# Kernel tuning notes

Measured on AMD Instinct MI355X. Metric: run time of the kernel, lower is better.

The kernel has to match this reference:

```python
import jax, jax.numpy as jnp
import numpy as np

B, C, W, H = 1024, 1, 128, 128
NUM_IDS = 64
MARGIN = 0.3


def setup_inputs() -> dict:
    key = jax.random.key(0)
    k1, k2 = jax.random.split(key)
    inputs = jax.random.normal(k1, (B, C, W, H), dtype=jnp.float32)
    targets = jax.random.randint(k2, (B,), 0, NUM_IDS, dtype=jnp.int32)
    return {"inputs": inputs, "targets": targets}


def _dc_align(anchor, other):
    # Batched cross-attention alignment (DCModuleOptimized assumption):
    # modi = softmax(anchor @ other^T / sqrt(h)) @ other, per sample.
    h = anchor.shape[-1]
    scale = 1.0 / jnp.sqrt(jnp.asarray(h, anchor.dtype))
    att = jax.nn.softmax(jnp.einsum('bij,bkj->bik', anchor, other) * scale, axis=-1)
    return jnp.einsum('bik,bkj->bij', att, other)


def reference(inputs, targets):
    b, c, w, h = inputs.shape
    x = inputs.reshape(b, -1)                      # (n, d); requires c == 1 downstream
    n = b
    # Pairwise Euclidean distances, stable clamp as in torch code
    sq = jnp.sum(x * x, axis=1)                    # (n,)
    dist = sq[:, None] + sq[None, :] - 2.0 * (x @ x.T)
    dist = jnp.sqrt(jnp.clip(dist, 1e-12, None))   # (n, n)
    mask = targets[:, None] == targets[None, :]    # (n, n) same-identity mask
    # Vectorized hard mining (replaces the per-row Python loop)
    NEG = jnp.asarray(-1e30, dist.dtype)
    POS = jnp.asarray(1e30, dist.dtype)
    hp_idx = jnp.argmax(jnp.where(mask, dist, NEG), axis=1)   # hardest positive per row
    hn_idx = jnp.argmin(jnp.where(mask, POS, dist), axis=1)   # hardest negative per row
    anchor = x.reshape(b, w, h)
    h_pos = anchor[hp_idx]                         # (b, w, h) gathered hard positives
    h_neg = anchor[hn_idx]                         # (b, w, h) gathered hard negatives
    # DC module applied over the whole batch at once
    modi_pos = _dc_align(anchor, h_pos)
    modi_neg = _dc_align(anchor, h_neg)
    dap = anchor.reshape(b, -1) - modi_pos.reshape(b, -1)
    dan = anchor.reshape(b, -1) - modi_neg.reshape(b, -1)
    dist_ap = jnp.sqrt(jnp.sum(dap * dap, axis=1))
    dist_an = jnp.sqrt(jnp.sum(dan * dan, axis=1))
    # MarginRankingLoss with y = 1: mean(relu(dist_ap - dist_an + margin))
    loss = jnp.mean(jax.nn.relu(dist_ap - dist_an + MARGIN))
    return loss
```

## Files before the change

kernel.cpp:

```cpp
#include <hip/hip_runtime.h>
#include <stdint.h>

#define NSAMP 1024
#define D 16384
#define WH 128
#define MARGIN 0.3f
#define SCALE 0.08838834764831845f
#define RSCALE 11.313708498984761f
#define MARG 0.03f
#define LISTCAP 2048

typedef unsigned int uint;
typedef unsigned short ushort_t;

typedef __attribute__((ext_vector_type(8))) short bf16x8;
typedef __attribute__((ext_vector_type(4))) float f32x4;

__device__ __forceinline__ float bf2f(unsigned short b) {
    return __uint_as_float(((uint)b) << 16);
}
__device__ __forceinline__ unsigned short f2bf(float f) {
    uint u = __float_as_uint(f);
    u += 0x7fffu + ((u >> 16) & 1u);
    return (unsigned short)(u >> 16);
}
__device__ __forceinline__ void gload_lds16(const void* g, void* l) {
    __builtin_amdgcn_global_load_lds(
        (const __attribute__((address_space(1))) uint32_t*)g,
        (__attribute__((address_space(3))) uint32_t*)l, 16, 0, 0);
}
__device__ __forceinline__ int lds_off(int row, int col) {
    return row * 256 + ((((col >> 3) ^ (row & 15)) << 4) | ((col & 7) << 1));
}

__global__ __launch_bounds__(256) void k_norms_hi(const float* __restrict__ x,
                                                  float* __restrict__ sq,
                                                  ushort_t* __restrict__ xhi) {
    int b = blockIdx.x;
    int tid = threadIdx.x;
    const float* xr = x + (size_t)b * D;
    ushort_t* hr = xhi + (size_t)b * D;
    float s = 0.f;
    #pragma unroll
    for (int m = 0; m < 16; ++m) {
        int e = m * 1024 + tid * 4;
        float4 v = *(const float4*)(xr + e);
        s += v.x * v.x + v.y * v.y + v.z * v.z + v.w * v.w;
        ushort4 h;
        h.x = f2bf(v.x); h.y = f2bf(v.y); h.z = f2bf(v.z); h.w = f2bf(v.w);
        *(ushort4*)(hr + e) = h;
    }
    for (int off = 32; off; off >>= 1) s += __shfl_down(s, off, 64);
    __shared__ float red[4];
    if ((tid & 63) == 0) red[tid >> 6] = s;
    __syncthreads();
    if (tid == 0) sq[b] = red[0] + red[1] + red[2] + red[3];
}

__global__ __launch_bounds__(256) void k_gram_hi(const ushort_t* __restrict__ xhi,
                                                 float* __restrict__ Gp,
                                                 int nks, int ksub) {
    int ks = blockIdx.x, bi = blockIdx.y, bj = blockIdx.z;
    int ti = bi < bj ? bi : bj;
    int tj = bi < bj ? bj : bi;
    bool diag = (bi == bj);
    int i0 = ti * 128, j0 = tj * 128;
    int kstart = ks * ksub + ((bi > bj) ? (ksub >> 1) : 0);
    int niter = diag ? (ksub >> 6) : (ksub >> 7);

    int tid = threadIdx.x;
    int w = tid >> 6, lane = tid & 63;
    int wm = w & 1, wn = w >> 1;
    int quad = lane >> 4, m16 = lane & 15;
    int srow = lane >> 2, sseg = lane & 3;
    int swseg = sseg ^ ((srow >> 1) & 3);
    int rsw = (quad ^ ((m16 >> 1) & 3)) << 3;

    __shared__ __align__(16) ushort_t A_s[2][128 * 32];
    __shared__ __align__(16) ushort_t B_s[2][128 * 32];

    f32x4 acc[4][4];
    #pragma unroll
    for (int ii = 0; ii < 4; ++ii)
        #pragma unroll
        for (int jj = 0; jj < 4; ++jj)
            acc[ii][jj] = (f32x4){0.f, 0.f, 0.f, 0.f};

    const size_t Abase = (size_t)i0 * D;
    const size_t Bbase = (size_t)j0 * D;

    for (int kb = 0; kb < niter; ++kb) {
        int k0 = kstart + kb * 64;
        #pragma unroll
        for (int kk = 0; kk < 2; ++kk) {
            #pragma unroll
            for (int c = 0; c < 2; ++c) {
                int r = w * 32 + c * 16 + srow;
                size_t go = (size_t)r * D + k0 + kk * 32 + swseg * 8;
                int lo = (w * 32 + c * 16) * 32;
                gload_lds16(xhi + Abase + go, &A_s[kk][lo]);
                gload_lds16(xhi + Bbase + go, &B_s[kk][lo]);
            }
        }
        __syncthreads();

        #pragma unroll
        for (int kk = 0; kk < 2; ++kk) {
            bf16x8 ah[4], bh[4];
            #pragma unroll
            for (int ii = 0; ii < 4; ++ii) {
                int ar = wm * 64 + ii * 16 + m16;
                ah[ii] = *(const bf16x8*)&A_s[kk][ar * 32 + rsw];
            }
            #pragma unroll
            for (int jj = 0; jj < 4; ++jj) {
                int br = wn * 64 + jj * 16 + m16;
                bh[jj] = *(const bf16x8*)&B_s[kk][br * 32 + rsw];
            }
            #pragma unroll
            for (int ii = 0; ii < 4; ++ii)
                #pragma unroll
                for (int jj = 0; jj < 4; ++jj)
                    acc[ii][jj] = __builtin_amdgcn_mfma_f32_16x16x32_bf16(ah[ii], bh[jj], acc[ii][jj], 0, 0, 0);
        }
        __syncthreads();
    }

    int slot;
    if (diag) {
        slot = bi * nks + ks;
    } else {
        int offidx = ti * 7 - (ti * (ti - 1)) / 2 + (tj - ti - 1);
        slot = 8 * nks + offidx * 2 * nks + 2 * ks + (bi > bj ? 1 : 0);
    }
    float* Gb = Gp + ((size_t)slot << 14);
    #pragma unroll
    for (int ii = 0; ii < 4; ++ii)
        #pragma unroll
        for (int jj = 0; jj < 4; ++jj) {
            int rg = wm * 64 + ii * 16 + quad * 4;
            int cg = wn * 64 + jj * 16 + m16;
            #pragma unroll
            for (int r = 0; r < 4; ++r)
                Gb[(rg + r) * 128 + cg] = acc[ii][jj][r];
        }
}

__global__ __launch_bounds__(256) void k_fold_tri(const float* __restrict__ Gp,
                                                  float* __restrict__ G, int nks,
                                                  int* __restrict__ cnt) {
    if (blockIdx.x == 0 && blockIdx.y == 0 && threadIdx.x == 0) cnt[0] = 0;
    int t = blockIdx.x;
    int panel = blockIdx.y;
    int bi = 0, rem = t;
    while (rem >= 8 - bi) { rem -= 8 - bi; ++bi; }
    int bj = bi + rem;
    bool diag = (bi == bj);
    int tid = threadIdx.x;

    int base_slot, nsl;
    if (diag) { base_slot = bi * nks; nsl = nks; }
    else {
        int offidx = bi * 7 - (bi * (bi - 1)) / 2 + (bj - bi - 1);
        base_slot = 8 * nks + offidx * 2 * nks; nsl = 2 * nks;
    }
    const float* P = Gp + (((size_t)base_slot) << 14) + panel * 4096;

    float4 s[4];
    #pragma unroll
    for (int m = 0; m < 4; ++m)
        s[m] = *(const float4*)(P + (tid + 256 * m) * 4);
    for (int p = 1; p < nsl; ++p) {
        const float* Pp = P + (((size_t)p) << 14);
        #pragma unroll
        for (int m = 0; m < 4; ++m) {
            float4 v = *(const float4*)(Pp + (tid + 256 * m) * 4);
            s[m].x += v.x; s[m].y += v.y; s[m].z += v.z; s[m].w += v.w;
        }
    }

    int i0 = bi * 128, j0 = bj * 128, r0 = panel * 32;
    __shared__ float ts[32][129];
    #pragma unroll
    for (int m = 0; m < 4; ++m) {
        int p4 = (tid + 256 * m) * 4;
        int lr = p4 >> 7, lc = p4 & 127;
        *(float4*)(&G[(size_t)(i0 + r0 + lr) * NSAMP + j0 + lc]) = s[m];
        if (!diag) {
            ts[lr][lc] = s[m].x; ts[lr][lc + 1] = s[m].y;
            ts[lr][lc + 2] = s[m].z; ts[lr][lc + 3] = s[m].w;
        }
    }
    if (diag) return;
    __syncthreads();
    int oc = tid >> 1, half = tid & 1;
    float4 o[4];
    #pragma unroll
    for (int k = 0; k < 4; ++k) {
        int rr = half * 16 + k * 4;
        o[k].x = ts[rr][oc]; o[k].y = ts[rr + 1][oc];
        o[k].z = ts[rr + 2][oc]; o[k].w = ts[rr + 3][oc];
    }
    float* Gm = &G[(size_t)(j0 + oc) * NSAMP + i0 + r0 + half * 16];
    #pragma unroll
    for (int k = 0; k < 4; ++k) *(float4*)(Gm + k * 4) = o[k];
}

__global__ void k_select_flag(const float* __restrict__ G,
                              const float* __restrict__ sq, const int* __restrict__ tgt,
                              int* __restrict__ hp, int* __restrict__ hn,
                              float* __restrict__ dsq, float* __restrict__ bestd,
                              int* __restrict__ list, int* __restrict__ cnt) {
    int i = blockIdx.x;
    int tid = threadIdx.x;
    float sqi = sq[i];
    int ti = tgt[i];
    float dloc[4]; bool sloc[4];
    float pv = -3.0e38f; int pj = 0x7FFFFFFF;
    float nv = 3.0e38f;  int nj = 0x7FFFFFFF;
    #pragma unroll
    for (int m = 0; m < 4; ++m) {
        int j = tid + 256 * m;
        float g = G[(size_t)i * NSAMP + j];
        float d = sqrtf(fmaxf(sqi + sq[j] - 2.f * g, 1e-12f));
        bool same = (tgt[j] == ti);
        dloc[m] = d; sloc[m] = same;
        float cp = same ? d : -1e30f;
        float cn = same ? 1e30f : d;
        if (cp > pv || (cp == pv && j < pj)) { pv = cp; pj = j; }
        if (cn < nv || (cn == nv && j < nj)) { nv = cn; nj = j; }
    }
    for (int off = 32; off; off >>= 1) {
        float opv = __shfl_down(pv, off, 64); int opj = __shfl_down(pj, off, 64);
        float onv = __shfl_down(nv, off, 64); int onj = __shfl_down(nj, off, 64);
        if (opv > pv || (opv == pv && opj < pj)) { pv = opv; pj = opj; }
        if (onv < nv || (onv == nv && onj < nj)) { nv = onv; nj = onj; }
    }
    __shared__ float spv[4], snv[4];
    __shared__ int spj[4], snj[4];
    __shared__ float bb[2];
    __shared__ int cc[2];
    if ((tid & 63) == 0) { int wv = tid >> 6; spv[wv] = pv; spj[wv] = pj; snv[wv] = nv; snj[wv] = nj; }
    __syncthreads();
    if (tid == 0) {
        for (int wv = 1; wv < 4; ++wv) {
            if (spv[wv] > pv || (spv[wv] == pv && spj[wv] < pj)) { pv = spv[wv]; pj = spj[wv]; }
            if (snv[wv] < nv || (snv[wv] == nv && snj[wv] < nj)) { nv = snv[wv]; nj = snj[wv]; }
        }
        hp[i] = pj; hn[i] = nj;
        dsq[i] = sqi; dsq[NSAMP + i] = sqi;
        bestd[i] = pv; bestd[NSAMP + i] = nv;
        bb[0] = pv; bb[1] = nv;
        cc[0] = 0; cc[1] = 0;
    }
    __syncthreads();
    float bp = bb[0], bn = bb[1];
    int lp = 0, ln = 0;
    #pragma unroll
    for (int m = 0; m < 4; ++m) {
        if (sloc[m] && dloc[m] >= bp - MARG) lp++;
        if (!sloc[m] && dloc[m] <= bn + MARG) ln++;
    }
    if (lp) atomicAdd(&cc[0], lp);
    if (ln) atomicAdd(&cc[1], ln);
    __syncthreads();
    if (tid == 0) {
        if (cc[0] > 1) { int k = atomicAdd(cnt, 1); if (k < LISTCAP) list[k] = i; }
        if (cc[1] > 1) { int k = atomicAdd(cnt, 1); if (k < LISTCAP) list[k] = i | (1 << 16); }
    }
}

__global__ __launch_bounds__(256) void k_fix(const float* __restrict__ G,
                                             const float* __restrict__ sq,
                                             const int* __restrict__ tgt,
                                             const float* __restrict__ x,
                                             const ushort_t* __restrict__ xhi,
                                             const float* __restrict__ bestd,
                                             const int* __restrict__ list,
                                             const int* __restrict__ cnt,
                                             int* __restrict__ hp, int* __restrict__ hn) {
    int n = cnt[0]; if (n > LISTCAP) n = LISTCAP;
    int tid = threadIdx.x;
    __shared__ int cand[32];
    __shared__ int ncand;
    __shared__ float bred[4];
    for (int e = blockIdx.x; e < n; e += gridDim.x) {
        int ent = list[e];
        int i = ent & 0xffff, type = ent >> 16;
        if (tid == 0) ncand = 0;
        __syncthreads();
        float bd = bestd[type * NSAMP + i];
        float sqi = sq[i];
        int ti = tgt[i];
        #pragma unroll
        for (int m = 0; m < 4; ++m) {
            int j = tid + 256 * m;
            float g = G[(size_t)i * NSAMP + j];
            float d = sqrtf(fmaxf(sqi + sq[j] - 2.f * g, 1e-12f));
            bool same = (tgt[j] == ti);
            bool fl = (type == 0) ? (same && d >= bd - MARG)
                                  : (!same && d <= bd + MARG);
            if (fl) { int k = atomicAdd(&ncand, 1); if (k < 32) cand[k] = j; }
        }
        __syncthreads();
        int nc = ncand < 32 ? ncand : 32;
        float bestv = (type == 0) ? -3.0e38f : 3.0e38f;
        int bestj = 0x7FFFFFFF;
        const float* xi = x + (size_t)i * D;
        const ushort_t* hi = xhi + (size_t)i * D;
        for (int c = 0; c < nc; ++c) {
            int j = cand[c];
            const float* xj = x + (size_t)j * D;
            const ushort_t* hj = xhi + (size_t)j * D;
            float corr = 0.f;
            #pragma unroll
            for (int m = 0; m < 16; ++m) {
                int k = m * 1024 + tid * 4;
                float4 xa = *(const float4*)(xi + k);
                float4 xb = *(const float4*)(xj + k);
                ushort4 ha = *(const ushort4*)(hi + k);
                ushort4 hb = *(const ushort4*)(hj + k);
                float a0 = bf2f(ha.x), a1 = bf2f(ha.y), a2 = bf2f(ha.z), a3 = bf2f(ha.w);
                float b0 = bf2f(hb.x), b1 = bf2f(hb.y), b2 = bf2f(hb.z), b3 = bf2f(hb.w);
                corr += a0 * (xb.x - b0) + (xa.x - a0) * b0;
                corr += a1 * (xb.y - b1) + (xa.y - a1) * b1;
                corr += a2 * (xb.z - b2) + (xa.z - a2) * b2;
                corr += a3 * (xb.w - b3) + (xa.w - a3) * b3;
            }
            for (int off = 32; off; off >>= 1) corr += __shfl_down(corr, off, 64);
            if ((tid & 63) == 0) bred[tid >> 6] = corr;
            __syncthreads();
            float cs = bred[0] + bred[1] + bred[2] + bred[3];
            float g = G[(size_t)i * NSAMP + j];
            float d2 = sqi + sq[j] - 2.f * (g + cs);
            float d = sqrtf(fmaxf(d2, 1e-12f));
            if (type == 0) {
                if (d > bestv || (d == bestv && j < bestj)) { bestv = d; bestj = j; }
            } else {
                if (d < bestv || (d == bestv && j < bestj)) { bestv = d; bestj = j; }
            }
            __syncthreads();
        }
        if (tid == 0 && nc > 0) { if (type == 0) hp[i] = bestj; else hn[i] = bestj; }
        __syncthreads();
    }
}

__global__ __launch_bounds__(256) void k_dc_mfma(const ushort_t* __restrict__ xhi,
                                                 const int* __restrict__ hp,
                                                 const int* __restrict__ hn,
                                                 float* __restrict__ dsq) {
    int b = blockIdx.x;
    int which = blockIdx.y;
    int q = blockIdx.z;
    int oidx = (which == 0) ? hp[b] : hn[b];
    const ushort_t* Ag = xhi + (size_t)b * D;
    const ushort_t* Og = xhi + (size_t)oidx * D;

    __shared__ __align__(16) char smem[32768];

    int tid = threadIdx.x;
    int wv = tid >> 6, lane = tid & 63;
    int quad = lane >> 4, m16 = lane & 15;
    int rt = q * 4 + wv;

    bf16x8 af[4];
    #pragma unroll
    for (int ks = 0; ks < 4; ++ks)
        af[ks] = *(const bf16x8*)(Ag + (rt * 16 + m16) * WH + ks * 32 + quad * 8);

    {
        uint4 stg[8];
        #pragma unroll
        for (int k = 0; k < 8; ++k)
            stg[k] = *(const uint4*)((const char*)Og + (size_t)(tid + 256 * k) * 16);
        #pragma unroll
        for (int k = 0; k < 8; ++k) {
            int g = tid + 256 * k;
            *(uint4*)(smem + lds_off(g >> 4, (g & 15) * 8)) = stg[k];
        }
    }
    __syncthreads();

    f32x4 acc[8];
    #pragma unroll
    for (int ti = 0; ti < 8; ++ti)
        acc[ti] = (f32x4){0.f, 0.f, 0.f, 0.f};
    #pragma unroll
    for (int ks = 0; ks < 4; ++ks) {
        bf16x8 of[8];
        #pragma unroll
        for (int ti = 0; ti < 8; ++ti)
            of[ti] = *(const bf16x8*)(smem + lds_off(ti * 16 + m16, (ks * 4 + quad) * 8));
        #pragma unroll
        for (int ti = 0; ti < 8; ++ti)
            acc[ti] = __builtin_amdgcn_mfma_f32_16x16x32_bf16(of[ti], af[ks], acc[ti], 0, 0, 0);
    }

    int c0 = (tid & 31) * 4, h0 = (tid >> 5) * 16;
    uint4 trd[4][2];
    #pragma unroll
    for (int j = 0; j < 4; ++j)
        #pragma unroll
        for (int k = 0; k < 2; ++k)
            trd[j][k] = *(const uint4*)(smem + lds_off(c0 + j, h0 + 8 * k));
    __syncthreads();

    #pragma unroll
    for (int i = 0; i < 16; ++i) {
        uint v[4];
        #pragma unroll
        for (int j = 0; j < 4; ++j) {
            uint wo = ((const uint*)&trd[j][i >> 3])[(i >> 1) & 3];
            v[j] = (i & 1) ? (wo >> 16) : (wo & 0xffffu);
        }
        uint2 pk;
        pk.x = v[0] | (v[1] << 16);
        pk.y = v[2] | (v[3] << 16);
        *(uint2*)(smem + lds_off(h0 + i, c0)) = pk;
    }

    float tpart = 0.f;
    bf16x8 pf[4];
    {
        float mx = -3.0e38f;
        #pragma unroll
        for (int ti = 0; ti < 8; ++ti)
            #pragma unroll
            for (int r = 0; r < 4; ++r) {
                float s = acc[ti][r] * SCALE;
                acc[ti][r] = s;
                mx = fmaxf(mx, s);
            }
        mx = fmaxf(mx, __shfl_xor(mx, 16, 64));
        mx = fmaxf(mx, __shfl_xor(mx, 32, 64));
        float sum = 0.f, tnum = 0.f;
        #pragma unroll
        for (int ti = 0; ti < 8; ++ti)
            #pragma unroll
            for (int r = 0; r < 4; ++r) {
                float s = acc[ti][r];
                float e = __expf(s - mx);
                acc[ti][r] = e;
                sum += e;
                tnum += s * e;
            }
        sum += __shfl_xor(sum, 16, 64);
        sum += __shfl_xor(sum, 32, 64);
        tnum += __shfl_xor(tnum, 16, 64);
        tnum += __shfl_xor(tnum, 32, 64);
        float inv = 1.f / sum;
        tpart = 0.25f * tnum * inv;

        uint Ep[8][2];
        #pragma unroll
        for (int ti = 0; ti < 8; ++ti) {
            Ep[ti][0] = (uint)f2bf(acc[ti][0] * inv) |
                        ((uint)f2bf(acc[ti][1] * inv) << 16);
            Ep[ti][1] = (uint)f2bf(acc[ti][2] * inv) |
                        ((uint)f2bf(acc[ti][3] * inv) << 16);
        }
        int tih = quad >> 1;
        #pragma unroll
        for (int ks = 0; ks < 4; ++ks) {
            union { uint u[4]; bf16x8 v; } fr;
            #pragma unroll
            for (int k = 0; k < 4; ++k) {
                int src = (((quad << 1) + (k >> 1)) & 3) * 16 + m16;
                int a = __shfl((int)Ep[2 * ks + 0][k & 1], src, 64);
                int bsh = __shfl((int)Ep[2 * ks + 1][k & 1], src, 64);
                fr.u[k] = (uint)((tih == 0) ? a : bsh);
            }
            pf[ks] = fr.v;
        }
    }
    __syncthreads();

    #pragma unroll
    for (int tj = 0; tj < 8; ++tj)
        acc[tj] = (f32x4){0.f, 0.f, 0.f, 0.f};
    #pragma unroll
    for (int ks = 0; ks < 4; ++ks) {
        bf16x8 otf[8];
        #pragma unroll
        for (int tj = 0; tj < 8; ++tj)
            otf[tj] = *(const bf16x8*)(smem + lds_off(tj * 16 + m16, (ks * 4 + quad) * 8));
        #pragma unroll
        for (int tj = 0; tj < 8; ++tj)
            acc[tj] = __builtin_amdgcn_mfma_f32_16x16x32_bf16(pf[ks], otf[tj], acc[tj], 0, 0, 0);
    }

    float m2 = 0.f;
    #pragma unroll
    for (int tj = 0; tj < 8; ++tj)
        #pragma unroll
        for (int r = 0; r < 4; ++r) {
            float mvv = acc[tj][r];
            m2 += mvv * mvv;
        }
    float part = m2 - 2.f * RSCALE * tpart;
    for (int off = 32; off; off >>= 1) part += __shfl_down(part, off, 64);
    if (lane == 0) atomicAdd(&dsq[which * NSAMP + b], part);
}

__global__ void k_loss(const float* __restrict__ dsq, float* __restrict__ out) {
    int tid = threadIdx.x;
    float s = 0.f;
    #pragma unroll
    for (int m = 0; m < 4; ++m) {
        int b = tid + 256 * m;
        float ap = sqrtf(fmaxf(dsq[b], 0.f));
        float an = sqrtf(fmaxf(dsq[NSAMP + b], 0.f));
        s += fmaxf(ap - an + MARGIN, 0.f);
    }
    for (int off = 32; off; off >>= 1) s += __shfl_down(s, off, 64);
    __shared__ float red[4];
    if ((tid & 63) == 0) red[tid >> 6] = s;
    __syncthreads();
    if (tid == 0) out[0] = (red[0] + red[1] + red[2] + red[3]) * (1.f / NSAMP);
}

extern "C" void kernel_launch(void* const* d_in, const int* in_sizes, int n_in,
                              void* d_out, int out_size, void* d_ws, size_t ws_size,
                              hipStream_t stream) {
    const float* x = (const float*)d_in[0];
    const int* tgt = (const int*)d_in[1];
    float* out = (float*)d_out;
    char* ws = (char*)d_ws;

    const size_t XB = (size_t)NSAMP * D * 2;
    const size_t GB1 = (size_t)NSAMP * NSAMP * 4;
    int nks = (ws_size >= 16 * GB1 + XB + GB1 + (size_t)65536) ? 16 : 8;

    float* Gp = (float*)ws;
    ushort_t* xhi = (ushort_t*)(ws + nks * GB1);
    float* G = (float*)(ws + nks * GB1 + XB);
    char* tail = ws + nks * GB1 + XB + GB1;
    float* sq = (float*)tail;
    float* dsq = sq + NSAMP;
    float* bestd = dsq + 2 * NSAMP;
    int* hp = (int*)(bestd + 2 * NSAMP);
    int* hn = hp + NSAMP;
    int* list = hn + NSAMP;
    int* cnt = list + LISTCAP;

    k_norms_hi<<<NSAMP, 256, 0, stream>>>(x, sq, xhi);
    k_gram_hi<<<dim3(nks, 8, 8), 256, 0, stream>>>(xhi, Gp, nks, D / nks);
    k_fold_tri<<<dim3(36, 4), 256, 0, stream>>>(Gp, G, nks, cnt);
    k_select_flag<<<NSAMP, 256, 0, stream>>>(G, sq, tgt, hp, hn, dsq, bestd, list, cnt);
    k_fix<<<64, 256, 0, stream>>>(G, sq, tgt, x, xhi, bestd, list, cnt, hp, hn);
    k_dc_mfma<<<dim3(NSAMP, 2, 2), 256, 0, stream>>>(xhi, hp, hn, dsq);
    k_loss<<<1, 256, 0, stream>>>(dsq, out);
}
```

Measured before the change: 221.1 us.

## Fuse hard-mining fix into select kernel and double-buffer triangular Gram tiles

The separate flag and fix kernels are merged: each row block now re-checks its own near-tie candidates in fp32-corrected precision using distances it already holds in registers. This drops the global work list, the atomic counter and one launch. The Gram kernel now launches only the 36 upper-triangle tiles with 16 K-splits instead of an 8x8 grid that split off-diagonal work in half. Its K loop is restructured into a 32-wide double-buffered pipeline that prefetches the next slice into LDS while the MFMAs run. The risk is that near-tie fixes now run serially inside 1024 blocks instead of being spread across 64 blocks, and the workspace layout assumes NKS=16 always fits.

```diff
diff --git a/kernel.cpp b/kernel.cpp
--- a/kernel.cpp
+++ b/kernel.cpp
@@ -8,7 +8,8 @@
 #define SCALE 0.08838834764831845f
 #define RSCALE 11.313708498984761f
 #define MARG 0.03f
-#define LISTCAP 2048
+#define NKS 16
+#define NTILE 36
 
 typedef unsigned int uint;
 typedef unsigned short ushort_t;
@@ -58,15 +59,14 @@
 }
 
 __global__ __launch_bounds__(256) void k_gram_hi(const ushort_t* __restrict__ xhi,
-                                                 float* __restrict__ Gp,
-                                                 int nks, int ksub) {
-    int ks = blockIdx.x, bi = blockIdx.y, bj = blockIdx.z;
-    int ti = bi < bj ? bi : bj;
-    int tj = bi < bj ? bj : bi;
-    bool diag = (bi == bj);
-    int i0 = ti * 128, j0 = tj * 128;
-    int kstart = ks * ksub + ((bi > bj) ? (ksub >> 1) : 0);
-    int niter = diag ? (ksub >> 6) : (ksub >> 7);
+                                                 float* __restrict__ Gp) {
+    int ks = blockIdx.x;
+    int t = blockIdx.y;
+    int bi = 0, rem = t;
+    while (rem >= 8 - bi) { rem -= 8 - bi; ++bi; }
+    int bj = bi + rem;
+    int i0 = bi * 128, j0 = bj * 128;
+    int kstart = ks * (D / NKS);
 
     int tid = threadIdx.x;
     int w = tid >> 6, lane = tid & 63;
@@ -89,51 +89,44 @@
     const size_t Abase = (size_t)i0 * D;
     const size_t Bbase = (size_t)j0 * D;
 
+    auto stage = [&](int bsel, int k0) {
+        #pragma unroll
+        for (int c = 0; c < 2; ++c) {
+            int r = w * 32 + c * 16 + srow;
+            size_t go = (size_t)r * D + k0 + swseg * 8;
+            int lo = (w * 32 + c * 16) * 32;
+            gload_lds16(xhi + Abase + go, &A_s[bsel][lo]);
+            gload_lds16(xhi + Bbase + go, &B_s[bsel][lo]);
+        }
+    };
+
+    stage(0, kstart);
+    __syncthreads();
+    int buf = 0;
+    const int niter = (D / NKS) / 32;
     for (int kb = 0; kb < niter; ++kb) {
-        int k0 = kstart + kb * 64;
-        #pragma unroll
-        for (int kk = 0; kk < 2; ++kk) {
+        if (kb < niter - 1) stage(buf ^ 1, kstart + (kb + 1) * 32);
+        bf16x8 ah[4], bh[4];
+        #pragma unroll
+        for (int ii = 0; ii < 4; ++ii) {
+            int ar = wm * 64 + ii * 16 + m16;
+            ah[ii] = *(const bf16x8*)&A_s[buf][ar * 32 + rsw];
+        }
+        #pragma unroll
+        for (int jj = 0; jj < 4; ++jj) {
+            int br = wn * 64 + jj * 16 + m16;
+            bh[jj] = *(const bf16x8*)&B_s[buf][br * 32 + rsw];
+        }
+        #pragma unroll
+        for (int ii = 0; ii < 4; ++ii)
             #pragma unroll
-            for (int c = 0; c < 2; ++c) {
-                int r = w * 32 + c * 16 + srow;
-                size_t go = (size_t)r * D + k0 + kk * 32 + swseg * 8;
-                int lo = (w * 32 + c * 16) * 32;
-                gload_lds16(xhi + Abase + go, &A_s[kk][lo]);
-                gload_lds16(xhi + Bbase + go, &B_s[kk][lo]);
-            }
-        }
+            for (int jj = 0; jj < 4; ++jj)
+                acc[ii][jj] = __builtin_amdgcn_mfma_f32_16x16x32_bf16(ah[ii], bh[jj], acc[ii][jj], 0, 0, 0);
         __syncthreads();
-
-        #pragma unroll
-        for (int kk = 0; kk < 2; ++kk) {
-            bf16x8 ah[4], bh[4];
-            #pragma unroll
-            for (int ii = 0; ii < 4; ++ii) {
-                int ar = wm * 64 + ii * 16 + m16;
-                ah[ii] = *(const bf16x8*)&A_s[kk][ar * 32 + rsw];
-            }
-            #pragma unroll
-            for (int jj = 0; jj < 4; ++jj) {
-                int br = wn * 64 + jj * 16 + m16;
-                bh[jj] = *(const bf16x8*)&B_s[kk][br * 32 + rsw];
-            }
-            #pragma unroll
-            for (int ii = 0; ii < 4; ++ii)
-                #pragma unroll
-                for (int jj = 0; jj < 4; ++jj)
-                    acc[ii][jj] = __builtin_amdgcn_mfma_f32_16x16x32_bf16(ah[ii], bh[jj], acc[ii][jj], 0, 0, 0);
-        }
-        __syncthreads();
-    }
-
-    int slot;
-    if (diag) {
-        slot = bi * nks + ks;
-    } else {
-        int offidx = ti * 7 - (ti * (ti - 1)) / 2 + (tj - ti - 1);
-        slot = 8 * nks + offidx * 2 * nks + 2 * ks + (bi > bj ? 1 : 0);
-    }
-    float* Gb = Gp + ((size_t)slot << 14);
+        buf ^= 1;
+    }
+
+    float* Gb = Gp + ((size_t)(t * NKS + ks) << 14);
     #pragma unroll
     for (int ii = 0; ii < 4; ++ii)
         #pragma unroll
@@ -147,9 +140,7 @@
 }
 
 __global__ __launch_bounds__(256) void k_fold_tri(const float* __restrict__ Gp,
-                                                  float* __restrict__ G, int nks,
-                                                  int* __restrict__ cnt) {
-    if (blockIdx.x == 0 && blockIdx.y == 0 && threadIdx.x == 0) cnt[0] = 0;
+                                                  float* __restrict__ G) {
     int t = blockIdx.x;
     int panel = blockIdx.y;
     int bi = 0, rem = t;
@@ -158,19 +149,14 @@
     bool diag = (bi == bj);
     int tid = threadIdx.x;
 
-    int base_slot, nsl;
-    if (diag) { base_slot = bi * nks; nsl = nks; }
-    else {
-        int offidx = bi * 7 - (bi * (bi - 1)) / 2 + (bj - bi - 1);
-        base_slot = 8 * nks + offidx * 2 * nks; nsl = 2 * nks;
-    }
-    const float* P = Gp + (((size_t)base_slot) << 14) + panel * 4096;
+    const float* P = Gp + (((size_t)t * NKS) << 14) + panel * 4096;
 
     float4 s[4];
     #pragma unroll
     for (int m = 0; m < 4; ++m)
         s[m] = *(const float4*)(P + (tid + 256 * m) * 4);
-    for (int p = 1; p < nsl; ++p) {
+    #pragma unroll
+    for (int p = 1; p < NKS; ++p) {
         const float* Pp = P + (((size_t)p) << 14);
         #pragma unroll
         for (int m = 0; m < 4; ++m) {
@@ -206,11 +192,14 @@
     for (int k = 0; k < 4; ++k) *(float4*)(Gm + k * 4) = o[k];
 }
 
-__global__ void k_select_flag(const float* __restrict__ G,
-                              const float* __restrict__ sq, const int* __restrict__ tgt,
-                              int* __restrict__ hp, int* __restrict__ hn,
-                              float* __restrict__ dsq, float* __restrict__ bestd,
-                              int* __restrict__ list, int* __restrict__ cnt) {
+__global__ __launch_bounds__(256) void k_select_fix(const float* __restrict__ G,
+                                                    const float* __restrict__ sq,
+                                                    const int* __restrict__ tgt,
+                                                    const float* __restrict__ x,
+                                                    const ushort_t* __restrict__ xhi,
+                                                    int* __restrict__ hp,
+                                                    int* __restrict__ hn,
+                                                    float* __restrict__ dsq) {
     int i = blockIdx.x;
     int tid = threadIdx.x;
     float sqi = sq[i];
@@ -249,65 +238,43 @@
         }
         hp[i] = pj; hn[i] = nj;
         dsq[i] = sqi; dsq[NSAMP + i] = sqi;
-        bestd[i] = pv; bestd[NSAMP + i] = nv;
         bb[0] = pv; bb[1] = nv;
         cc[0] = 0; cc[1] = 0;
     }
     __syncthreads();
-    float bp = bb[0], bn = bb[1];
-    int lp = 0, ln = 0;
-    #pragma unroll
-    for (int m = 0; m < 4; ++m) {
-        if (sloc[m] && dloc[m] >= bp - MARG) lp++;
-        if (!sloc[m] && dloc[m] <= bn + MARG) ln++;
-    }
-    if (lp) atomicAdd(&cc[0], lp);
-    if (ln) atomicAdd(&cc[1], ln);
-    __syncthreads();
-    if (tid == 0) {
-        if (cc[0] > 1) { int k = atomicAdd(cnt, 1); if (k < LISTCAP) list[k] = i; }
-        if (cc[1] > 1) { int k = atomicAdd(cnt, 1); if (k < LISTCAP) list[k] = i | (1 << 16); }
-    }
-}
-
-__global__ __launch_bounds__(256) void k_fix(const float* __restrict__ G,
-                                             const float* __restrict__ sq,
-                                             const int* __restrict__ tgt,
-                                             const float* __restrict__ x,
-                                             const ushort_t* __restrict__ xhi,
-                                             const float* __restrict__ bestd,
-                                             const int* __restrict__ list,
-                                             const int* __restrict__ cnt,
-                                             int* __restrict__ hp, int* __restrict__ hn) {
-    int n = cnt[0]; if (n > LISTCAP) n = LISTCAP;
-    int tid = threadIdx.x;
+    {
+        int lp = 0, ln = 0;
+        #pragma unroll
+        for (int m = 0; m < 4; ++m) {
+            if (sloc[m] && dloc[m] >= bb[0] - MARG) lp++;
+            if (!sloc[m] && dloc[m] <= bb[1] + MARG) ln++;
+        }
+        if (lp) atomicAdd(&cc[0], lp);
+        if (ln) atomicAdd(&cc[1], ln);
+    }
+    __syncthreads();
+
     __shared__ int cand[32];
     __shared__ int ncand;
     __shared__ float bred[4];
-    for (int e = blockIdx.x; e < n; e += gridDim.x) {
-        int ent = list[e];
-        int i = ent & 0xffff, type = ent >> 16;
+    const float* xi = x + (size_t)i * D;
+    const ushort_t* hi = xhi + (size_t)i * D;
+    for (int type = 0; type < 2; ++type) {
+        if (cc[type] <= 1) continue;
         if (tid == 0) ncand = 0;
         __syncthreads();
-        float bd = bestd[type * NSAMP + i];
-        float sqi = sq[i];
-        int ti = tgt[i];
+        float bd = bb[type];
         #pragma unroll
         for (int m = 0; m < 4; ++m) {
             int j = tid + 256 * m;
-            float g = G[(size_t)i * NSAMP + j];
-            float d = sqrtf(fmaxf(sqi + sq[j] - 2.f * g, 1e-12f));
-            bool same = (tgt[j] == ti);
-            bool fl = (type == 0) ? (same && d >= bd - MARG)
-                                  : (!same && d <= bd + MARG);
+            bool fl = (type == 0) ? (sloc[m] && dloc[m] >= bd - MARG)
+                                  : (!sloc[m] && dloc[m] <= bd + MARG);
             if (fl) { int k = atomicAdd(&ncand, 1); if (k < 32) cand[k] = j; }
         }
         __syncthreads();
         int nc = ncand < 32 ? ncand : 32;
         float bestv = (type == 0) ? -3.0e38f : 3.0e38f;
         int bestj = 0x7FFFFFFF;
-        const float* xi = x + (size_t)i * D;
-        const ushort_t* hi = xhi + (size_t)i * D;
         for (int c = 0; c < nc; ++c) {
             int j = cand[c];
             const float* xj = x + (size_t)j * D;
@@ -528,27 +495,23 @@
     float* out = (float*)d_out;
     char* ws = (char*)d_ws;
 
+    const size_t GPB = (size_t)NTILE * NKS * 65536;
     const size_t XB = (size_t)NSAMP * D * 2;
     const size_t GB1 = (size_t)NSAMP * NSAMP * 4;
-    int nks = (ws_size >= 16 * GB1 + XB + GB1 + (size_t)65536) ? 16 : 8;
 
     float* Gp = (float*)ws;
-    ushort_t* xhi = (ushort_t*)(ws + nks * GB1);
-    float* G = (float*)(ws + nks * GB1 + XB);
-    char* tail = ws + nks * GB1 + XB + GB1;
+    ushort_t* xhi = (ushort_t*)(ws + GPB);
+    float* G = (float*)(ws + GPB + XB);
+    char* tail = ws + GPB + XB + GB1;
     float* sq = (float*)tail;
     float* dsq = sq + NSAMP;
-    float* bestd = dsq + 2 * NSAMP;
-    int* hp = (int*)(bestd + 2 * NSAMP);
+    int* hp = (int*)(dsq + 2 * NSAMP);
     int* hn = hp + NSAMP;
-    int* list = hn + NSAMP;
-    int* cnt = list + LISTCAP;
 
     k_norms_hi<<<NSAMP, 256, 0, stream>>>(x, sq, xhi);
-    k_gram_hi<<<dim3(nks, 8, 8), 256, 0, stream>>>(xhi, Gp, nks, D / nks);
-    k_fold_tri<<<dim3(36, 4), 256, 0, stream>>>(Gp, G, nks, cnt);
-    k_select_flag<<<NSAMP, 256, 0, stream>>>(G, sq, tgt, hp, hn, dsq, bestd, list, cnt);
-    k_fix<<<64, 256, 0, stream>>>(G, sq, tgt, x, xhi, bestd, list, cnt, hp, hn);
+    k_gram_hi<<<dim3(NKS, NTILE), 256, 0, stream>>>(xhi, Gp);
+    k_fold_tri<<<dim3(NTILE, 4), 256, 0, stream>>>(Gp, G);
+    k_select_fix<<<NSAMP, 256, 0, stream>>>(G, sq, tgt, x, xhi, hp, hn, dsq);
     k_dc_mfma<<<dim3(NSAMP, 2, 2), 256, 0, stream>>>(xhi, hp, hn, dsq);
     k_loss<<<1, 256, 0, stream>>>(dsq, out);
 }
```

Result: faster. 196.2 us (-11.3%).
